# Performance work log

Measured on AMD Instinct MI355X. Metric: run time of the kernel, lower is better.

Reference implementation:

```python
import jax, jax.numpy as jnp
import numpy as np

HID = 32
NUM_GRAPHS = 256
N_NODES = 100000


def graph_conv(x, src, dst, ew, rel_w, rel_b, root_w):
    # PyG GraphConv: out = lin_rel(sum_{j in N(i)} e_ji * x_j) + lin_root(x_i)
    msg = x[src] * ew[:, None]                                  # [E, F] gather
    agg = jax.ops.segment_sum(msg, dst, num_segments=N_NODES)    # [N, F] scatter-add
    return agg @ rel_w + rel_b + x @ root_w


def setup_inputs() -> dict:
    key = jax.random.key(0)
    ks = jax.random.split(key, 16)
    N, E, F = N_NODES, 1600000, 64
    x = jax.random.normal(ks[0], (N, F), dtype=jnp.float32)
    edge_index = jax.random.randint(ks[1], (2, E), 0, N, dtype=jnp.int64)
    edge_attr = jax.random.uniform(ks[2], (E,), dtype=jnp.float32)
    batch = jnp.sort(jax.random.randint(ks[3], (N,), 0, NUM_GRAPHS, dtype=jnp.int64))
    s = lambda k, shp: jax.random.normal(k, shp, dtype=jnp.float32) * 0.1
    return {
        "x": x, "edge_index": edge_index, "edge_attr": edge_attr, "batch": batch,
        "conv1_rel_w": s(ks[4], (F, HID)), "conv1_rel_b": jnp.zeros((HID,), jnp.float32),
        "conv1_root_w": s(ks[5], (F, HID)),
        "conv2_rel_w": s(ks[6], (HID, HID)), "conv2_rel_b": jnp.zeros((HID,), jnp.float32),
        "conv2_root_w": s(ks[7], (HID, HID)),
        "lin1_w": s(ks[8], (HID, 32)), "lin1_b": jnp.zeros((32,), jnp.float32),
        "lin2_w": s(ks[9], (32, 16)), "lin2_b": jnp.zeros((16,), jnp.float32),
        "lin_w": s(ks[10], (16, 1)), "lin_b": jnp.zeros((1,), jnp.float32),
    }


def reference(x, edge_index, edge_attr, batch,
              conv1_rel_w, conv1_rel_b, conv1_root_w,
              conv2_rel_w, conv2_rel_b, conv2_root_w,
              lin1_w, lin1_b, lin2_w, lin2_b, lin_w, lin_b):
    src, dst = edge_index[0], edge_index[1]
    h = jax.nn.relu(graph_conv(x, src, dst, edge_attr, conv1_rel_w, conv1_rel_b, conv1_root_w))
    h = jax.nn.relu(graph_conv(h, src, dst, edge_attr, conv2_rel_w, conv2_rel_b, conv2_root_w))
    # global mean pool over graphs
    sums = jax.ops.segment_sum(h, batch, num_segments=NUM_GRAPHS)          # [G, 32]
    cnts = jax.ops.segment_sum(jnp.ones((h.shape[0],), h.dtype), batch, num_segments=NUM_GRAPHS)
    g = sums / jnp.maximum(cnts, 1.0)[:, None]
    # dropout is identity in eval mode
    g = jax.nn.relu(g @ lin1_w + lin1_b)
    g = g @ lin2_w + lin2_b
    g = jax.nn.relu(g)
    return g @ lin_w + lin_b  # [G, 1]
```

## Files before the change

kernel.cpp:

```cpp
#include <hip/hip_runtime.h>
#include <hip/hip_fp16.h>

#define NGRAPH 256
#define FIN 64
#define HID 32
#define NB_SHIFT 8
#define NB_NODES 256
#define KMAX2 512
#define EPB 2048
#define EPT 8
#define NT 64
#define XPAD 65
#define HPAD 33

__global__ __launch_bounds__(256, 4) void node_lin64(
    const float* __restrict__ x, const float* __restrict__ Wrel,
    const float* __restrict__ Wroot, const float* __restrict__ bias,
    __half* __restrict__ A, float* __restrict__ B, int N)
{
    __shared__ float sWr[FIN * HID];
    __shared__ float sWo[FIN * HID];
    __shared__ float sb[HID];
    __shared__ float sx[NT * XPAD];
    int tid = threadIdx.x;
    {
        const float4* Wr4 = (const float4*)Wrel;
        const float4* Wo4 = (const float4*)Wroot;
        for (int i = tid; i < FIN * HID / 4; i += 256) {
            ((float4*)sWr)[i] = Wr4[i];
            ((float4*)sWo)[i] = Wo4[i];
        }
        if (tid < HID) sb[tid] = bias[tid];
    }
    int base = blockIdx.x * NT;
    {
        const float4* x4 = (const float4*)x;
        for (int i = tid; i < NT * 16; i += 256) {
            int row = i >> 4, c4 = i & 15;
            int n = base + row;
            float4 v = (n < N) ? x4[(size_t)n * 16 + c4]
                               : make_float4(0.f, 0.f, 0.f, 0.f);
            *(float4*)&sx[row * XPAD + c4 * 4] = v;
        }
    }
    __syncthreads();

    int nl = tid >> 3;
    int fq = (tid & 7) * 4;
    const float* xa = &sx[nl * XPAD];
    const float* xb = &sx[(nl + 32) * XPAD];
    float4 ar0 = make_float4(0.f,0.f,0.f,0.f), ao0 = ar0;
    float4 ar1 = ar0, ao1 = ar0;
    #pragma unroll 4
    for (int k = 0; k < FIN; ++k) {
        float4 w4 = *(const float4*)&sWr[k * HID + fq];
        float4 o4 = *(const float4*)&sWo[k * HID + fq];
        float va = xa[k], vb = xb[k];
        ar0.x = fmaf(va, w4.x, ar0.x); ar0.y = fmaf(va, w4.y, ar0.y);
        ar0.z = fmaf(va, w4.z, ar0.z); ar0.w = fmaf(va, w4.w, ar0.w);
        ao0.x = fmaf(va, o4.x, ao0.x); ao0.y = fmaf(va, o4.y, ao0.y);
        ao0.z = fmaf(va, o4.z, ao0.z); ao0.w = fmaf(va, o4.w, ao0.w);
        ar1.x = fmaf(vb, w4.x, ar1.x); ar1.y = fmaf(vb, w4.y, ar1.y);
        ar1.z = fmaf(vb, w4.z, ar1.z); ar1.w = fmaf(vb, w4.w, ar1.w);
        ao1.x = fmaf(vb, o4.x, ao1.x); ao1.y = fmaf(vb, o4.y, ao1.y);
        ao1.z = fmaf(vb, o4.z, ao1.z); ao1.w = fmaf(vb, o4.w, ao1.w);
    }
    float4 bb = *(const float4*)&sb[fq];
    int n0 = base + nl, n1 = base + nl + 32;
    if (n0 < N) {
        __half2 pa = __floats2half2_rn(ar0.x, ar0.y);
        __half2 pb = __floats2half2_rn(ar0.z, ar0.w);
        uint2 pk; pk.x = *(unsigned*)&pa; pk.y = *(unsigned*)&pb;
        *(uint2*)&A[(size_t)n0 * HID + fq] = pk;
        ao0.x += bb.x; ao0.y += bb.y; ao0.z += bb.z; ao0.w += bb.w;
        *(float4*)&B[(size_t)n0 * HID + fq] = ao0;
    }
    if (n1 < N) {
        __half2 pa = __floats2half2_rn(ar1.x, ar1.y);
        __half2 pb = __floats2half2_rn(ar1.z, ar1.w);
        uint2 pk; pk.x = *(unsigned*)&pa; pk.y = *(unsigned*)&pb;
        *(uint2*)&A[(size_t)n1 * HID + fq] = pk;
        ao1.x += bb.x; ao1.y += bb.y; ao1.z += bb.z; ao1.w += bb.w;
        *(float4*)&B[(size_t)n1 * HID + fq] = ao1;
    }
}

__global__ __launch_bounds__(256, 4) void node_lin32(
    const float* __restrict__ Hpre, const float* __restrict__ Wrel,
    const float* __restrict__ Wroot, const float* __restrict__ bias,
    __half* __restrict__ A, float* __restrict__ C, int N)
{
    __shared__ float sWr[HID * HID];
    __shared__ float sWo[HID * HID];
    __shared__ float sb[HID];
    __shared__ float sh[NT * HPAD];
    int tid = threadIdx.x;
    {
        const float4* Wr4 = (const float4*)Wrel;
        const float4* Wo4 = (const float4*)Wroot;
        for (int i = tid; i < HID * HID / 4; i += 256) {
            ((float4*)sWr)[i] = Wr4[i];
            ((float4*)sWo)[i] = Wo4[i];
        }
        if (tid < HID) sb[tid] = bias[tid];
    }
    int base = blockIdx.x * NT;
    {
        const float4* H4 = (const float4*)Hpre;
        for (int i = tid; i < NT * 8; i += 256) {
            int row = i >> 3, c4 = i & 7;
            int n = base + row;
            float4 v = make_float4(0.f, 0.f, 0.f, 0.f);
            if (n < N) {
                v = H4[(size_t)n * 8 + c4];
                v.x = v.x > 0.f ? v.x : 0.f; v.y = v.y > 0.f ? v.y : 0.f;
                v.z = v.z > 0.f ? v.z : 0.f; v.w = v.w > 0.f ? v.w : 0.f;
            }
            *(float4*)&sh[row * HPAD + c4 * 4] = v;
        }
    }
    __syncthreads();

    int nl = tid >> 3;
    int fq = (tid & 7) * 4;
    const float* xa = &sh[nl * HPAD];
    const float* xb = &sh[(nl + 32) * HPAD];
    float4 ar0 = make_float4(0.f,0.f,0.f,0.f), ao0 = ar0;
    float4 ar1 = ar0, ao1 = ar0;
    #pragma unroll 4
    for (int k = 0; k < HID; ++k) {
        float4 w4 = *(const float4*)&sWr[k * HID + fq];
        float4 o4 = *(const float4*)&sWo[k * HID + fq];
        float va = xa[k], vb = xb[k];
        ar0.x = fmaf(va, w4.x, ar0.x); ar0.y = fmaf(va, w4.y, ar0.y);
        ar0.z = fmaf(va, w4.z, ar0.z); ar0.w = fmaf(va, w4.w, ar0.w);
        ao0.x = fmaf(va, o4.x, ao0.x); ao0.y = fmaf(va, o4.y, ao0.y);
        ao0.z = fmaf(va, o4.z, ao0.z); ao0.w = fmaf(va, o4.w, ao0.w);
        ar1.x = fmaf(vb, w4.x, ar1.x); ar1.y = fmaf(vb, w4.y, ar1.y);
        ar1.z = fmaf(vb, w4.z, ar1.z); ar1.w = fmaf(vb, w4.w, ar1.w);
        ao1.x = fmaf(vb, o4.x, ao1.x); ao1.y = fmaf(vb, o4.y, ao1.y);
        ao1.z = fmaf(vb, o4.z, ao1.z); ao1.w = fmaf(vb, o4.w, ao1.w);
    }
    float4 bb = *(const float4*)&sb[fq];
    int n0 = base + nl, n1 = base + nl + 32;
    if (n0 < N) {
        __half2 pa = __floats2half2_rn(ar0.x, ar0.y);
        __half2 pb = __floats2half2_rn(ar0.z, ar0.w);
        uint2 pk; pk.x = *(unsigned*)&pa; pk.y = *(unsigned*)&pb;
        *(uint2*)&A[(size_t)n0 * HID + fq] = pk;
        ao0.x += bb.x; ao0.y += bb.y; ao0.z += bb.z; ao0.w += bb.w;
        *(float4*)&C[(size_t)n0 * HID + fq] = ao0;
    }
    if (n1 < N) {
        __half2 pa = __floats2half2_rn(ar1.x, ar1.y);
        __half2 pb = __floats2half2_rn(ar1.z, ar1.w);
        uint2 pk; pk.x = *(unsigned*)&pa; pk.y = *(unsigned*)&pb;
        *(uint2*)&A[(size_t)n1 * HID + fq] = pk;
        ao1.x += bb.x; ao1.y += bb.y; ao1.z += bb.z; ao1.w += bb.w;
        *(float4*)&C[(size_t)n1 * HID + fq] = ao1;
    }
}


__global__ __launch_bounds__(256) void bucket_hist(
    const int* __restrict__ dst, int* __restrict__ cbb, int E, int K, int NBLK)
{
    __shared__ int h[KMAX2];
    int tid = threadIdx.x;
    for (int i = tid; i < K; i += 256) h[i] = 0;
    __syncthreads();
    int e0 = blockIdx.x * EPB + tid * 8;
    if (e0 + 7 < E) {
        int4 d0 = *reinterpret_cast<const int4*>(dst + e0);
        int4 d1 = *reinterpret_cast<const int4*>(dst + e0 + 4);
        atomicAdd(&h[d0.x >> NB_SHIFT], 1); atomicAdd(&h[d0.y >> NB_SHIFT], 1);
        atomicAdd(&h[d0.z >> NB_SHIFT], 1); atomicAdd(&h[d0.w >> NB_SHIFT], 1);
        atomicAdd(&h[d1.x >> NB_SHIFT], 1); atomicAdd(&h[d1.y >> NB_SHIFT], 1);
        atomicAdd(&h[d1.z >> NB_SHIFT], 1); atomicAdd(&h[d1.w >> NB_SHIFT], 1);
    } else {
        for (int e = e0; e < E && e < e0 + 8; ++e)
            atomicAdd(&h[dst[e] >> NB_SHIFT], 1);
    }
    __syncthreads();
    for (int i = tid; i < K; i += 256)
        cbb[(size_t)i * NBLK + blockIdx.x] = h[i];
}

__global__ __launch_bounds__(256) void bucket_scan(
    int* __restrict__ cbb, int* __restrict__ btot, int NBLK)
{
    __shared__ int sc[256];
    size_t row = (size_t)blockIdx.x * NBLK;
    int t = threadIdx.x;
    int base = t * 4;
    int v[4]; int s = 0;
    #pragma unroll
    for (int j = 0; j < 4; ++j) { v[j] = (base + j < NBLK) ? cbb[row + base + j] : 0; s += v[j]; }
    sc[t] = s;
    __syncthreads();
    int acc = s;
    for (int off = 1; off < 256; off <<= 1) {
        int add = (t >= off) ? sc[t - off] : 0;
        __syncthreads();
        acc += add;
        sc[t] = acc;
        __syncthreads();
    }
    int run = acc - s;
    #pragma unroll
    for (int j = 0; j < 4; ++j) {
        if (base + j < NBLK) cbb[row + base + j] = run;
        run += v[j];
    }
    if (t == 255) btot[blockIdx.x] = acc;
}

__global__ __launch_bounds__(256) void btot_scan(
    const int* __restrict__ btot, int* __restrict__ bbase, int K)
{
    __shared__ int sc[256];
    int t = threadIdx.x;
    int base = t * 4;
    int v[4]; int s = 0;
    #pragma unroll
    for (int j = 0; j < 4; ++j) { v[j] = (base + j < K) ? btot[base + j] : 0; s += v[j]; }
    sc[t] = s;
    __syncthreads();
    int acc = s;
    for (int off = 1; off < 256; off <<= 1) {
        int add = (t >= off) ? sc[t - off] : 0;
        __syncthreads();
        acc += add;
        sc[t] = acc;
        __syncthreads();
    }
    int run = acc - s;
    #pragma unroll
    for (int j = 0; j < 4; ++j) {
        if (base + j < K) bbase[base + j] = run;
        run += v[j];
    }
    if (t == 255) bbase[K] = acc;
}

__global__ __launch_bounds__(256) void partB(
    const int* __restrict__ src, const int* __restrict__ dst,
    const float* __restrict__ ew, const int* __restrict__ cbb,
    const int* __restrict__ bbase, int2* __restrict__ stg8,
    int E, int K, int NBLK)
{
    __shared__ int4 pay[EPB];
    __shared__ int h[KMAX2];
    __shared__ int lofs[KMAX2];
    __shared__ int gb[KMAX2];
    __shared__ int sc[256];
    int tid = threadIdx.x;
    for (int i = tid; i < K; i += 256) h[i] = 0;
    __syncthreads();

    int base = blockIdx.x * EPB;
    int es[EPT], ds[EPT]; float wsr[EPT];
    #pragma unroll
    for (int k = 0; k < EPT; ++k) {
        int e = base + k * 256 + tid;
        if (e < E) {
            es[k] = src[e]; ds[k] = dst[e]; wsr[k] = ew[e];
            atomicAdd(&h[ds[k] >> NB_SHIFT], 1);
        } else ds[k] = -1;
    }
    __syncthreads();

    int b0 = tid * 2;
    int v0 = (b0 < K) ? h[b0] : 0;
    int v1 = (b0 + 1 < K) ? h[b0 + 1] : 0;
    int s = v0 + v1;
    sc[tid] = s;
    __syncthreads();
    int acc = s;
    for (int off = 1; off < 256; off <<= 1) {
        int add = (tid >= off) ? sc[tid - off] : 0;
        __syncthreads();
        acc += add;
        sc[tid] = acc;
        __syncthreads();
    }
    int run = acc - s;
    if (b0 < K) lofs[b0] = run;
    if (b0 + 1 < K) lofs[b0 + 1] = run + v0;
    __syncthreads();

    for (int b = tid; b < K; b += 256) {
        gb[b] = bbase[b] + cbb[(size_t)b * NBLK + blockIdx.x];
        h[b] = lofs[b];
    }
    __syncthreads();

    #pragma unroll
    for (int k = 0; k < EPT; ++k) {
        if (ds[k] >= 0) {
            int b = ds[k] >> NB_SHIFT;
            int dloc = ds[k] & (NB_NODES - 1);
            int slot = atomicAdd(&h[b], 1);
            pay[slot] = make_int4(es[k] | (dloc << 17), __float_as_int(wsr[k]),
                                  gb[b] + slot - lofs[b], 0);
        }
    }
    __syncthreads();

    int tot = E - base; if (tot > EPB) tot = EPB;
    for (int i = tid; i < tot; i += 256) {
        int4 p = pay[i];
        stg8[p.z] = make_int2(p.x, p.y);
    }
}

__global__ __launch_bounds__(512) void partC2(
    const int2* __restrict__ stg8, const int* __restrict__ bbase,
    int* __restrict__ rowptr, int2* __restrict__ perm, int N, int K)
{
    __shared__ int hcnt[NB_NODES];
    __shared__ int hinc[NB_NODES];
    int b = blockIdx.x;
    int n0 = b << NB_SHIFT;
    int nTop = n0 + NB_NODES; if (nTop > N) nTop = N;
    int nloc = nTop - n0;
    int tid = threadIdx.x;
    if (tid < NB_NODES) hcnt[tid] = 0;
    __syncthreads();
    int lo = bbase[b], hi = bbase[b + 1];
    for (int e = lo + tid; e < hi; e += 512)
        atomicAdd(&hcnt[stg8[e].x >> 17], 1);
    __syncthreads();
    if (tid < NB_NODES) hinc[tid] = hcnt[tid];
    __syncthreads();
    for (int off = 1; off < NB_NODES; off <<= 1) {
        int v = (tid < NB_NODES && tid >= off) ? hinc[tid - off] : 0;
        __syncthreads();
        if (tid < NB_NODES) hinc[tid] += v;
        __syncthreads();
    }
    if (tid < nloc) {
        int excl = hinc[tid] - hcnt[tid];
        rowptr[n0 + tid] = lo + excl;
        hcnt[tid] = excl;
    }
    if (b == K - 1 && tid == 0) rowptr[N] = hi;
    __syncthreads();
    for (int e = lo + tid; e < hi; e += 512) {
        int2 p = stg8[e];
        int pos = lo + atomicAdd(&hcnt[p.x >> 17], 1);
        perm[pos] = make_int2(p.x & 0x1FFFF, p.y);
    }
}

__global__ __launch_bounds__(256) void csr_agg(
    const int* __restrict__ rowptr, const int2* __restrict__ perm,
    const __half* __restrict__ A, float* __restrict__ out, int N)
{
    int gid = blockIdx.x * 256 + threadIdx.x;
    int n = gid >> 6;
    if (n >= N) return;
    int lane = threadIdx.x & 63;
    int slot = lane >> 3;
    int q = lane & 7;
    int e0 = rowptr[n], e1 = rowptr[n + 1];
    const uint2* A2 = (const uint2*)A;
    float4 a0 = make_float4(0.f, 0.f, 0.f, 0.f);
    float4 a1 = make_float4(0.f, 0.f, 0.f, 0.f);
    int e = e0 + slot;
    for (; e + 8 < e1; e += 16) {
        int2 p0 = perm[e];
        int2 p1 = perm[e + 8];
        uint2 r0 = A2[(size_t)p0.x * 8 + q];
        uint2 r1 = A2[(size_t)p1.x * 8 + q];
        float w0 = __int_as_float(p0.y), w1 = __int_as_float(p1.y);
        float2 f01 = __half22float2(*(__half2*)&r0.x);
        float2 f23 = __half22float2(*(__half2*)&r0.y);
        float2 g01 = __half22float2(*(__half2*)&r1.x);
        float2 g23 = __half22float2(*(__half2*)&r1.y);
        a0.x = fmaf(f01.x, w0, a0.x); a0.y = fmaf(f01.y, w0, a0.y);
        a0.z = fmaf(f23.x, w0, a0.z); a0.w = fmaf(f23.y, w0, a0.w);
        a1.x = fmaf(g01.x, w1, a1.x); a1.y = fmaf(g01.y, w1, a1.y);
        a1.z = fmaf(g23.x, w1, a1.z); a1.w = fmaf(g23.y, w1, a1.w);
    }
    for (; e < e1; e += 8) {
        int2 p = perm[e];
        uint2 r = A2[(size_t)p.x * 8 + q];
        float w = __int_as_float(p.y);
        float2 f01 = __half22float2(*(__half2*)&r.x);
        float2 f23 = __half22float2(*(__half2*)&r.y);
        a0.x = fmaf(f01.x, w, a0.x); a0.y = fmaf(f01.y, w, a0.y);
        a0.z = fmaf(f23.x, w, a0.z); a0.w = fmaf(f23.y, w, a0.w);
    }
    a0.x += a1.x; a0.y += a1.y; a0.z += a1.z; a0.w += a1.w;
    #pragma unroll
    for (int off = 8; off < 64; off <<= 1) {
        a0.x += __shfl_xor(a0.x, off, 64);
        a0.y += __shfl_xor(a0.y, off, 64);
        a0.z += __shfl_xor(a0.z, off, 64);
        a0.w += __shfl_xor(a0.w, off, 64);
    }
    if (lane < 8) {
        float4* O4 = (float4*)out;
        size_t oi = (size_t)n * 8 + q;
        float4 o = O4[oi];
        o.x += a0.x; o.y += a0.y; o.z += a0.z; o.w += a0.w;
        O4[oi] = o;
    }
}

__global__ __launch_bounds__(256) void pool_mlp(
    const float* __restrict__ C, const int* __restrict__ batch, int N,
    const float* __restrict__ W1, const float* __restrict__ b1,
    const float* __restrict__ W2, const float* __restrict__ b2,
    const float* __restrict__ W3, const float* __restrict__ b3,
    float* __restrict__ out)
{
    int g = blockIdx.x;
    int tid = threadIdx.x;
    int lo, hi;
    {
        int l = 0, r = N;
        while (l < r) { int m = (l + r) >> 1; if (batch[m] < g) l = m + 1; else r = m; }
        lo = l;
        r = N;
        while (l < r) { int m = (l + r) >> 1; if (batch[m] < g + 1) l = m + 1; else r = m; }
        hi = l;
    }
    __shared__ float ssum[8][32];
    __shared__ float gvec[32];
    __shared__ float h1v[32];
    __shared__ float h2v[16];
    int f = tid & 31, seg = tid >> 5;
    float acc = 0.f;
    for (int n = lo + seg; n < hi; n += 8) {
        float v = C[(size_t)n * HID + f];
        acc += v > 0.f ? v : 0.f;
    }
    ssum[seg][f] = acc;
    __syncthreads();
    if (tid < 32) {
        float s = 0.f;
        #pragma unroll
        for (int k = 0; k < 8; ++k) s += ssum[k][tid];
        float c = (float)(hi - lo); c = c > 1.f ? c : 1.f;
        gvec[tid] = s / c;
    }
    __syncthreads();
    if (tid < 32) {
        float a = b1[tid];
        #pragma unroll
        for (int k = 0; k < 32; ++k) a = fmaf(gvec[k], W1[k * 32 + tid], a);
        h1v[tid] = a > 0.f ? a : 0.f;
    }
    __syncthreads();
    if (tid < 16) {
        float a = b2[tid];
        #pragma unroll
        for (int k = 0; k < 32; ++k) a = fmaf(h1v[k], W2[k * 16 + tid], a);
        h2v[tid] = a > 0.f ? a : 0.f;
    }
    __syncthreads();
    if (tid == 0) {
        float o = b3[0];
        #pragma unroll
        for (int k = 0; k < 16; ++k) o = fmaf(h2v[k], W3[k], o);
        out[g] = o;
    }
}

extern "C" void kernel_launch(void* const* d_in, const int* in_sizes, int n_in,
                              void* d_out, int out_size, void* d_ws, size_t ws_size,
                              hipStream_t stream) {
    const float* x     = (const float*)d_in[0];
    const int*   ei    = (const int*)d_in[1];
    const float* ew    = (const float*)d_in[2];
    const int*   batch = (const int*)d_in[3];
    const float* c1rw  = (const float*)d_in[4];
    const float* c1rb  = (const float*)d_in[5];
    const float* c1ow  = (const float*)d_in[6];
    const float* c2rw  = (const float*)d_in[7];
    const float* c2rb  = (const float*)d_in[8];
    const float* c2ow  = (const float*)d_in[9];
    const float* l1w   = (const float*)d_in[10];
    const float* l1b   = (const float*)d_in[11];
    const float* l2w   = (const float*)d_in[12];
    const float* l2b   = (const float*)d_in[13];
    const float* lw    = (const float*)d_in[14];
    const float* lb    = (const float*)d_in[15];

    int N = in_sizes[0] / FIN;
    int E = in_sizes[2];
    const int* src = ei;
    const int* dst = ei + E;
    int K    = (N + NB_NODES - 1) >> NB_SHIFT;
    int NBLK = (E + EPB - 1) / EPB;

    char* ws = (char*)d_ws;
    size_t off = 0;
    auto alloc = [&](size_t nbytes) { void* p = ws + off; off += (nbytes + 255) & ~size_t(255); return p; };
    __half* A     = (__half*)alloc((size_t)N * HID * 2);
    float*  BC    = (float*) alloc((size_t)N * HID * 4);
    int2*   perm  = (int2*)  alloc((size_t)E * 8);
    int*   rowptr = (int*)   alloc((size_t)(N + 1) * 4);
    int*   btot   = (int*)   alloc((size_t)KMAX2 * 4);
    int*   bbase  = (int*)   alloc((size_t)(KMAX2 + 1) * 4);
    int*   cbb    = (int*)A;
    int2*  stg8   = (int2*)BC;

    int nb_node = (N + NT - 1) / NT;
    int nb_agg  = (int)(((long long)N * 64 + 255) / 256);

    bucket_hist<<<NBLK, 256, 0, stream>>>(dst, cbb, E, K, NBLK);
    bucket_scan<<<K, 256, 0, stream>>>(cbb, btot, NBLK);
    btot_scan<<<1, 256, 0, stream>>>(btot, bbase, K);
    partB<<<NBLK, 256, 0, stream>>>(src, dst, ew, cbb, bbase, stg8, E, K, NBLK);
    partC2<<<K, 512, 0, stream>>>(stg8, bbase, rowptr, perm, N, K);

    node_lin64<<<nb_node, 256, 0, stream>>>(x, c1rw, c1ow, c1rb, A, BC, N);
    csr_agg<<<nb_agg, 256, 0, stream>>>(rowptr, perm, A, BC, N);
    node_lin32<<<nb_node, 256, 0, stream>>>(BC, c2rw, c2ow, c2rb, A, BC, N);
    csr_agg<<<nb_agg, 256, 0, stream>>>(rowptr, perm, A, BC, N);
    pool_mlp<<<NGRAPH, 256, 0, stream>>>(BC, batch, N, l1w, l1b, l2w, l2b, lw, lb,
                                         (float*)d_out);
}
```

Before: 173.4 us.

## Fuse layer-1 aggregation with layer-2 node linear and stage partC2 buckets in LDS

Measured after the change: 176.6 us. About the same (+1.8%).

```diff
diff --git a/kernel.cpp b/kernel.cpp
--- a/kernel.cpp
+++ b/kernel.cpp
@@ -11,7 +11,7 @@
 #define EPT 8
 #define NT 64
 #define XPAD 65
-#define HPAD 33
+#define PCAP 6016
 
 __global__ __launch_bounds__(256, 4) void node_lin64(
     const float* __restrict__ x, const float* __restrict__ Wrel,
@@ -85,82 +85,6 @@
     }
 }
 
-__global__ __launch_bounds__(256, 4) void node_lin32(
-    const float* __restrict__ Hpre, const float* __restrict__ Wrel,
-    const float* __restrict__ Wroot, const float* __restrict__ bias,
-    __half* __restrict__ A, float* __restrict__ C, int N)
-{
-    __shared__ float sWr[HID * HID];
-    __shared__ float sWo[HID * HID];
-    __shared__ float sb[HID];
-    __shared__ float sh[NT * HPAD];
-    int tid = threadIdx.x;
-    {
-        const float4* Wr4 = (const float4*)Wrel;
-        const float4* Wo4 = (const float4*)Wroot;
-        for (int i = tid; i < HID * HID / 4; i += 256) {
-            ((float4*)sWr)[i] = Wr4[i];
-            ((float4*)sWo)[i] = Wo4[i];
-        }
-        if (tid < HID) sb[tid] = bias[tid];
-    }
-    int base = blockIdx.x * NT;
-    {
-        const float4* H4 = (const float4*)Hpre;
-        for (int i = tid; i < NT * 8; i += 256) {
-            int row = i >> 3, c4 = i & 7;
-            int n = base + row;
-            float4 v = make_float4(0.f, 0.f, 0.f, 0.f);
-            if (n < N) {
-                v = H4[(size_t)n * 8 + c4];
-                v.x = v.x > 0.f ? v.x : 0.f; v.y = v.y > 0.f ? v.y : 0.f;
-                v.z = v.z > 0.f ? v.z : 0.f; v.w = v.w > 0.f ? v.w : 0.f;
-            }
-            *(float4*)&sh[row * HPAD + c4 * 4] = v;
-        }
-    }
-    __syncthreads();
-
-    int nl = tid >> 3;
-    int fq = (tid & 7) * 4;
-    const float* xa = &sh[nl * HPAD];
-    const float* xb = &sh[(nl + 32) * HPAD];
-    float4 ar0 = make_float4(0.f,0.f,0.f,0.f), ao0 = ar0;
-    float4 ar1 = ar0, ao1 = ar0;
-    #pragma unroll 4
-    for (int k = 0; k < HID; ++k) {
-        float4 w4 = *(const float4*)&sWr[k * HID + fq];
-        float4 o4 = *(const float4*)&sWo[k * HID + fq];
-        float va = xa[k], vb = xb[k];
-        ar0.x = fmaf(va, w4.x, ar0.x); ar0.y = fmaf(va, w4.y, ar0.y);
-        ar0.z = fmaf(va, w4.z, ar0.z); ar0.w = fmaf(va, w4.w, ar0.w);
-        ao0.x = fmaf(va, o4.x, ao0.x); ao0.y = fmaf(va, o4.y, ao0.y);
-        ao0.z = fmaf(va, o4.z, ao0.z); ao0.w = fmaf(va, o4.w, ao0.w);
-        ar1.x = fmaf(vb, w4.x, ar1.x); ar1.y = fmaf(vb, w4.y, ar1.y);
-        ar1.z = fmaf(vb, w4.z, ar1.z); ar1.w = fmaf(vb, w4.w, ar1.w);
-        ao1.x = fmaf(vb, o4.x, ao1.x); ao1.y = fmaf(vb, o4.y, ao1.y);
-        ao1.z = fmaf(vb, o4.z, ao1.z); ao1.w = fmaf(vb, o4.w, ao1.w);
-    }
-    float4 bb = *(const float4*)&sb[fq];
-    int n0 = base + nl, n1 = base + nl + 32;
-    if (n0 < N) {
-        __half2 pa = __floats2half2_rn(ar0.x, ar0.y);
-        __half2 pb = __floats2half2_rn(ar0.z, ar0.w);
-        uint2 pk; pk.x = *(unsigned*)&pa; pk.y = *(unsigned*)&pb;
-        *(uint2*)&A[(size_t)n0 * HID + fq] = pk;
-        ao0.x += bb.x; ao0.y += bb.y; ao0.z += bb.z; ao0.w += bb.w;
-        *(float4*)&C[(size_t)n0 * HID + fq] = ao0;
-    }
-    if (n1 < N) {
-        __half2 pa = __floats2half2_rn(ar1.x, ar1.y);
-        __half2 pb = __floats2half2_rn(ar1.z, ar1.w);
-        uint2 pk; pk.x = *(unsigned*)&pa; pk.y = *(unsigned*)&pb;
-        *(uint2*)&A[(size_t)n1 * HID + fq] = pk;
-        ao1.x += bb.x; ao1.y += bb.y; ao1.z += bb.z; ao1.w += bb.w;
-        *(float4*)&C[(size_t)n1 * HID + fq] = ao1;
-    }
-}
-
 
 __global__ __launch_bounds__(256) void bucket_hist(
     const int* __restrict__ dst, int* __restrict__ cbb, int E, int K, int NBLK)
@@ -318,6 +242,7 @@
     const int2* __restrict__ stg8, const int* __restrict__ bbase,
     int* __restrict__ rowptr, int2* __restrict__ perm, int N, int K)
 {
+    __shared__ int2 pe[PCAP];
     __shared__ int hcnt[NB_NODES];
     __shared__ int hinc[NB_NODES];
     int b = blockIdx.x;
@@ -326,10 +251,20 @@
     int nloc = nTop - n0;
     int tid = threadIdx.x;
     if (tid < NB_NODES) hcnt[tid] = 0;
-    __syncthreads();
     int lo = bbase[b], hi = bbase[b + 1];
-    for (int e = lo + tid; e < hi; e += 512)
-        atomicAdd(&hcnt[stg8[e].x >> 17], 1);
+    int sz = hi - lo;
+    bool fit = (sz <= PCAP);
+    if (fit) {
+        for (int i = tid; i < sz; i += 512) pe[i] = stg8[lo + i];
+    }
+    __syncthreads();
+    if (fit) {
+        for (int i = tid; i < sz; i += 512)
+            atomicAdd(&hcnt[pe[i].x >> 17], 1);
+    } else {
+        for (int e = lo + tid; e < hi; e += 512)
+            atomicAdd(&hcnt[stg8[e].x >> 17], 1);
+    }
     __syncthreads();
     if (tid < NB_NODES) hinc[tid] = hcnt[tid];
     __syncthreads();
@@ -346,10 +281,113 @@
     }
     if (b == K - 1 && tid == 0) rowptr[N] = hi;
     __syncthreads();
-    for (int e = lo + tid; e < hi; e += 512) {
-        int2 p = stg8[e];
-        int pos = lo + atomicAdd(&hcnt[p.x >> 17], 1);
-        perm[pos] = make_int2(p.x & 0x1FFFF, p.y);
+    if (fit) {
+        for (int i = tid; i < sz; i += 512) {
+            int2 p = pe[i];
+            int pos = lo + atomicAdd(&hcnt[p.x >> 17], 1);
+            perm[pos] = make_int2(p.x & 0x1FFFF, p.y);
+        }
+    } else {
+        for (int e = lo + tid; e < hi; e += 512) {
+            int2 p = stg8[e];
+            int pos = lo + atomicAdd(&hcnt[p.x >> 17], 1);
+            perm[pos] = make_int2(p.x & 0x1FFFF, p.y);
+        }
+    }
+}
+
+__global__ __launch_bounds__(256) void csr_agg_lin32(
+    const int* __restrict__ rowptr, const int2* __restrict__ perm,
+    const __half* __restrict__ A1, const float* __restrict__ Bbase,
+    const float* __restrict__ W2rel, const float* __restrict__ W2root,
+    const float* __restrict__ b2,
+    __half* __restrict__ A2, float* __restrict__ C2base, int N)
+{
+    __shared__ float sWr[HID * HID];
+    __shared__ float sWo[HID * HID];
+    __shared__ float sb2[HID];
+    __shared__ float hrow[4][HID];
+    int tid = threadIdx.x;
+    {
+        const float4* Wr4 = (const float4*)W2rel;
+        const float4* Wo4 = (const float4*)W2root;
+        for (int i = tid; i < HID * HID / 4; i += 256) {
+            ((float4*)sWr)[i] = Wr4[i];
+            ((float4*)sWo)[i] = Wo4[i];
+        }
+        if (tid < HID) sb2[tid] = b2[tid];
+    }
+    __syncthreads();
+
+    int gid = blockIdx.x * 256 + tid;
+    int n = gid >> 6;
+    int w = tid >> 6;
+    int lane = tid & 63;
+    bool active = (n < N);
+
+    float4 a0 = make_float4(0.f, 0.f, 0.f, 0.f);
+    float4 a1 = make_float4(0.f, 0.f, 0.f, 0.f);
+    int slot = lane >> 3, q = lane & 7;
+    if (active) {
+        int e0 = rowptr[n], e1 = rowptr[n + 1];
+        const uint2* A2p = (const uint2*)A1;
+        int e = e0 + slot;
+        for (; e + 8 < e1; e += 16) {
+            int2 p0 = perm[e];
+            int2 p1 = perm[e + 8];
+            uint2 r0 = A2p[(size_t)p0.x * 8 + q];
+            uint2 r1 = A2p[(size_t)p1.x * 8 + q];
+            float w0 = __int_as_float(p0.y), w1 = __int_as_float(p1.y);
+            float2 f01 = __half22float2(*(__half2*)&r0.x);
+            float2 f23 = __half22float2(*(__half2*)&r0.y);
+            float2 g01 = __half22float2(*(__half2*)&r1.x);
+            float2 g23 = __half22float2(*(__half2*)&r1.y);
+            a0.x = fmaf(f01.x, w0, a0.x); a0.y = fmaf(f01.y, w0, a0.y);
+            a0.z = fmaf(f23.x, w0, a0.z); a0.w = fmaf(f23.y, w0, a0.w);
+            a1.x = fmaf(g01.x, w1, a1.x); a1.y = fmaf(g01.y, w1, a1.y);
+            a1.z = fmaf(g23.x, w1, a1.z); a1.w = fmaf(g23.y, w1, a1.w);
+        }
+        for (; e < e1; e += 8) {
+            int2 p = perm[e];
+            uint2 r = A2p[(size_t)p.x * 8 + q];
+            float wv = __int_as_float(p.y);
+            float2 f01 = __half22float2(*(__half2*)&r.x);
+            float2 f23 = __half22float2(*(__half2*)&r.y);
+            a0.x = fmaf(f01.x, wv, a0.x); a0.y = fmaf(f01.y, wv, a0.y);
+            a0.z = fmaf(f23.x, wv, a0.z); a0.w = fmaf(f23.y, wv, a0.w);
+        }
+        a0.x += a1.x; a0.y += a1.y; a0.z += a1.z; a0.w += a1.w;
+        #pragma unroll
+        for (int off = 8; off < 64; off <<= 1) {
+            a0.x += __shfl_xor(a0.x, off, 64);
+            a0.y += __shfl_xor(a0.y, off, 64);
+            a0.z += __shfl_xor(a0.z, off, 64);
+            a0.w += __shfl_xor(a0.w, off, 64);
+        }
+        if (lane < 8) {
+            float4 o = ((const float4*)Bbase)[(size_t)n * 8 + q];
+            o.x += a0.x; o.y += a0.y; o.z += a0.z; o.w += a0.w;
+            o.x = o.x > 0.f ? o.x : 0.f; o.y = o.y > 0.f ? o.y : 0.f;
+            o.z = o.z > 0.f ? o.z : 0.f; o.w = o.w > 0.f ? o.w : 0.f;
+            *(float4*)&hrow[w][q * 4] = o;
+        }
+    }
+    __syncthreads();
+    if (active) {
+        int f = lane & 31;
+        bool isRel = lane < 32;
+        const float* W = isRel ? sWr : sWo;
+        float a = isRel ? 0.f : sb2[f];
+        #pragma unroll 8
+        for (int k4 = 0; k4 < HID; k4 += 4) {
+            float4 h4 = *(const float4*)&hrow[w][k4];
+            a = fmaf(h4.x, W[(k4 + 0) * HID + f], a);
+            a = fmaf(h4.y, W[(k4 + 1) * HID + f], a);
+            a = fmaf(h4.z, W[(k4 + 2) * HID + f], a);
+            a = fmaf(h4.w, W[(k4 + 3) * HID + f], a);
+        }
+        if (isRel) A2[((size_t)n << 5) + f] = __float2half(a);
+        else       C2base[((size_t)n << 5) + f] = a;
     }
 }
 
@@ -499,13 +537,14 @@
     char* ws = (char*)d_ws;
     size_t off = 0;
     auto alloc = [&](size_t nbytes) { void* p = ws + off; off += (nbytes + 255) & ~size_t(255); return p; };
-    __half* A     = (__half*)alloc((size_t)N * HID * 2);
+    __half* A1    = (__half*)alloc((size_t)N * HID * 2);
+    __half* A2    = (__half*)alloc((size_t)N * HID * 2);
     float*  BC    = (float*) alloc((size_t)N * HID * 4);
     int2*   perm  = (int2*)  alloc((size_t)E * 8);
     int*   rowptr = (int*)   alloc((size_t)(N + 1) * 4);
     int*   btot   = (int*)   alloc((size_t)KMAX2 * 4);
     int*   bbase  = (int*)   alloc((size_t)(KMAX2 + 1) * 4);
-    int*   cbb    = (int*)A;
+    int*   cbb    = (int*)A1;
     int2*  stg8   = (int2*)BC;
 
     int nb_node = (N + NT - 1) / NT;
@@ -517,10 +556,10 @@
     partB<<<NBLK, 256, 0, stream>>>(src, dst, ew, cbb, bbase, stg8, E, K, NBLK);
     partC2<<<K, 512, 0, stream>>>(stg8, bbase, rowptr, perm, N, K);
 
-    node_lin64<<<nb_node, 256, 0, stream>>>(x, c1rw, c1ow, c1rb, A, BC, N);
-    csr_agg<<<nb_agg, 256, 0, stream>>>(rowptr, perm, A, BC, N);
-    node_lin32<<<nb_node, 256, 0, stream>>>(BC, c2rw, c2ow, c2rb, A, BC, N);
-    csr_agg<<<nb_agg, 256, 0, stream>>>(rowptr, perm, A, BC, N);
+    node_lin64<<<nb_node, 256, 0, stream>>>(x, c1rw, c1ow, c1rb, A1, BC, N);
+    csr_agg_lin32<<<nb_agg, 256, 0, stream>>>(rowptr, perm, A1, BC,
+                                              c2rw, c2ow, c2rb, A2, BC, N);
+    csr_agg<<<nb_agg, 256, 0, stream>>>(rowptr, perm, A2, BC, N);
     pool_mlp<<<NGRAPH, 256, 0, stream>>>(BC, batch, N, l1w, l1b, l2w, l2b, lw, lb,
                                          (float*)d_out);
 }
```

## Stage bucket edges in LDS for partC2 and widen csr_agg gathers to 16 bytes

Applied to the files above, without the earlier changes.

After: 177.5 us. +2.3%, slower.

```diff
diff --git a/kernel.cpp b/kernel.cpp
--- a/kernel.cpp
+++ b/kernel.cpp
@@ -12,6 +12,7 @@
 #define NT 64
 #define XPAD 65
 #define HPAD 33
+#define PCAP 6016
 
 __global__ __launch_bounds__(256, 4) void node_lin64(
     const float* __restrict__ x, const float* __restrict__ Wrel,
@@ -318,6 +319,7 @@
     const int2* __restrict__ stg8, const int* __restrict__ bbase,
     int* __restrict__ rowptr, int2* __restrict__ perm, int N, int K)
 {
+    __shared__ int2 pe[PCAP];
     __shared__ int hcnt[NB_NODES];
     __shared__ int hinc[NB_NODES];
     int b = blockIdx.x;
@@ -326,10 +328,20 @@
     int nloc = nTop - n0;
     int tid = threadIdx.x;
     if (tid < NB_NODES) hcnt[tid] = 0;
-    __syncthreads();
     int lo = bbase[b], hi = bbase[b + 1];
-    for (int e = lo + tid; e < hi; e += 512)
-        atomicAdd(&hcnt[stg8[e].x >> 17], 1);
+    int sz = hi - lo;
+    bool fit = (sz <= PCAP);
+    if (fit) {
+        for (int i = tid; i < sz; i += 512) pe[i] = stg8[lo + i];
+    }
+    __syncthreads();
+    if (fit) {
+        for (int i = tid; i < sz; i += 512)
+            atomicAdd(&hcnt[pe[i].x >> 17], 1);
+    } else {
+        for (int e = lo + tid; e < hi; e += 512)
+            atomicAdd(&hcnt[stg8[e].x >> 17], 1);
+    }
     __syncthreads();
     if (tid < NB_NODES) hinc[tid] = hcnt[tid];
     __syncthreads();
@@ -346,10 +358,18 @@
     }
     if (b == K - 1 && tid == 0) rowptr[N] = hi;
     __syncthreads();
-    for (int e = lo + tid; e < hi; e += 512) {
-        int2 p = stg8[e];
-        int pos = lo + atomicAdd(&hcnt[p.x >> 17], 1);
-        perm[pos] = make_int2(p.x & 0x1FFFF, p.y);
+    if (fit) {
+        for (int i = tid; i < sz; i += 512) {
+            int2 p = pe[i];
+            int pos = lo + atomicAdd(&hcnt[p.x >> 17], 1);
+            perm[pos] = make_int2(p.x & 0x1FFFF, p.y);
+        }
+    } else {
+        for (int e = lo + tid; e < hi; e += 512) {
+            int2 p = stg8[e];
+            int pos = lo + atomicAdd(&hcnt[p.x >> 17], 1);
+            perm[pos] = make_int2(p.x & 0x1FFFF, p.y);
+        }
     }
 }
 
@@ -361,51 +381,65 @@
     int n = gid >> 6;
     if (n >= N) return;
     int lane = threadIdx.x & 63;
-    int slot = lane >> 3;
-    int q = lane & 7;
+    int slot = lane >> 2;
+    int q = lane & 3;
     int e0 = rowptr[n], e1 = rowptr[n + 1];
-    const uint2* A2 = (const uint2*)A;
-    float4 a0 = make_float4(0.f, 0.f, 0.f, 0.f);
-    float4 a1 = make_float4(0.f, 0.f, 0.f, 0.f);
+    const uint4* A4 = (const uint4*)A;
+    float a0[8] = {0.f,0.f,0.f,0.f,0.f,0.f,0.f,0.f};
+    float a1[8] = {0.f,0.f,0.f,0.f,0.f,0.f,0.f,0.f};
     int e = e0 + slot;
-    for (; e + 8 < e1; e += 16) {
+    for (; e + 16 < e1; e += 32) {
         int2 p0 = perm[e];
-        int2 p1 = perm[e + 8];
-        uint2 r0 = A2[(size_t)p0.x * 8 + q];
-        uint2 r1 = A2[(size_t)p1.x * 8 + q];
+        int2 p1 = perm[e + 16];
+        uint4 r0 = A4[(size_t)p0.x * 4 + q];
+        uint4 r1 = A4[(size_t)p1.x * 4 + q];
         float w0 = __int_as_float(p0.y), w1 = __int_as_float(p1.y);
-        float2 f01 = __half22float2(*(__half2*)&r0.x);
-        float2 f23 = __half22float2(*(__half2*)&r0.y);
-        float2 g01 = __half22float2(*(__half2*)&r1.x);
-        float2 g23 = __half22float2(*(__half2*)&r1.y);
-        a0.x = fmaf(f01.x, w0, a0.x); a0.y = fmaf(f01.y, w0, a0.y);
-        a0.z = fmaf(f23.x, w0, a0.z); a0.w = fmaf(f23.y, w0, a0.w);
-        a1.x = fmaf(g01.x, w1, a1.x); a1.y = fmaf(g01.y, w1, a1.y);
-        a1.z = fmaf(g23.x, w1, a1.z); a1.w = fmaf(g23.y, w1, a1.w);
-    }
-    for (; e < e1; e += 8) {
+        float2 c0 = __half22float2(*(__half2*)&r0.x);
+        float2 c1 = __half22float2(*(__half2*)&r0.y);
+        float2 c2 = __half22float2(*(__half2*)&r0.z);
+        float2 c3 = __half22float2(*(__half2*)&r0.w);
+        a0[0] = fmaf(c0.x, w0, a0[0]); a0[1] = fmaf(c0.y, w0, a0[1]);
+        a0[2] = fmaf(c1.x, w0, a0[2]); a0[3] = fmaf(c1.y, w0, a0[3]);
+        a0[4] = fmaf(c2.x, w0, a0[4]); a0[5] = fmaf(c2.y, w0, a0[5]);
+        a0[6] = fmaf(c3.x, w0, a0[6]); a0[7] = fmaf(c3.y, w0, a0[7]);
+        float2 d0 = __half22float2(*(__half2*)&r1.x);
+        float2 d1 = __half22float2(*(__half2*)&r1.y);
+        float2 d2 = __half22float2(*(__half2*)&r1.z);
+        float2 d3 = __half22float2(*(__half2*)&r1.w);
+        a1[0] = fmaf(d0.x, w1, a1[0]); a1[1] = fmaf(d0.y, w1, a1[1]);
+        a1[2] = fmaf(d1.x, w1, a1[2]); a1[3] = fmaf(d1.y, w1, a1[3]);
+        a1[4] = fmaf(d2.x, w1, a1[4]); a1[5] = fmaf(d2.y, w1, a1[5]);
+        a1[6] = fmaf(d3.x, w1, a1[6]); a1[7] = fmaf(d3.y, w1, a1[7]);
+    }
+    for (; e < e1; e += 16) {
         int2 p = perm[e];
-        uint2 r = A2[(size_t)p.x * 8 + q];
+        uint4 r = A4[(size_t)p.x * 4 + q];
         float w = __int_as_float(p.y);
-        float2 f01 = __half22float2(*(__half2*)&r.x);
-        float2 f23 = __half22float2(*(__half2*)&r.y);
-        a0.x = fmaf(f01.x, w, a0.x); a0.y = fmaf(f01.y, w, a0.y);
-        a0.z = fmaf(f23.x, w, a0.z); a0.w = fmaf(f23.y, w, a0.w);
-    }
-    a0.x += a1.x; a0.y += a1.y; a0.z += a1.z; a0.w += a1.w;
-    #pragma unroll
-    for (int off = 8; off < 64; off <<= 1) {
-        a0.x += __shfl_xor(a0.x, off, 64);
-        a0.y += __shfl_xor(a0.y, off, 64);
-        a0.z += __shfl_xor(a0.z, off, 64);
-        a0.w += __shfl_xor(a0.w, off, 64);
-    }
-    if (lane < 8) {
+        float2 c0 = __half22float2(*(__half2*)&r.x);
+        float2 c1 = __half22float2(*(__half2*)&r.y);
+        float2 c2 = __half22float2(*(__half2*)&r.z);
+        float2 c3 = __half22float2(*(__half2*)&r.w);
+        a0[0] = fmaf(c0.x, w, a0[0]); a0[1] = fmaf(c0.y, w, a0[1]);
+        a0[2] = fmaf(c1.x, w, a0[2]); a0[3] = fmaf(c1.y, w, a0[3]);
+        a0[4] = fmaf(c2.x, w, a0[4]); a0[5] = fmaf(c2.y, w, a0[5]);
+        a0[6] = fmaf(c3.x, w, a0[6]); a0[7] = fmaf(c3.y, w, a0[7]);
+    }
+    #pragma unroll
+    for (int i = 0; i < 8; ++i) a0[i] += a1[i];
+    #pragma unroll
+    for (int off = 4; off < 64; off <<= 1) {
+        #pragma unroll
+        for (int i = 0; i < 8; ++i) a0[i] += __shfl_xor(a0[i], off, 64);
+    }
+    if (lane < 4) {
         float4* O4 = (float4*)out;
-        size_t oi = (size_t)n * 8 + q;
+        size_t oi = (size_t)n * 8 + q * 2;
         float4 o = O4[oi];
-        o.x += a0.x; o.y += a0.y; o.z += a0.z; o.w += a0.w;
+        o.x += a0[0]; o.y += a0[1]; o.z += a0[2]; o.w += a0[3];
         O4[oi] = o;
+        float4 p = O4[oi + 1];
+        p.x += a0[4]; p.y += a0[5]; p.z += a0[6]; p.w += a0[7];
+        O4[oi + 1] = p;
     }
 }
 
```

## Split fp16 gather table into two feature halves and stage bucket in LDS

Applied to the files above, without the earlier changes.

After: 274.2 us. 1.58x slower.

```diff
diff --git a/kernel.cpp b/kernel.cpp
--- a/kernel.cpp
+++ b/kernel.cpp
@@ -12,6 +12,8 @@
 #define NT 64
 #define XPAD 65
 #define HPAD 33
+#define PCAP 6016
+
 
 __global__ __launch_bounds__(256, 4) void node_lin64(
     const float* __restrict__ x, const float* __restrict__ Wrel,
@@ -66,12 +68,14 @@
         ao1.z = fmaf(vb, o4.z, ao1.z); ao1.w = fmaf(vb, o4.w, ao1.w);
     }
     float4 bb = *(const float4*)&sb[fq];
+    size_t tOff = (fq < 16) ? (size_t)0 : (size_t)N * 16;
+    int fl = fq & 15;
     int n0 = base + nl, n1 = base + nl + 32;
     if (n0 < N) {
         __half2 pa = __floats2half2_rn(ar0.x, ar0.y);
         __half2 pb = __floats2half2_rn(ar0.z, ar0.w);
         uint2 pk; pk.x = *(unsigned*)&pa; pk.y = *(unsigned*)&pb;
-        *(uint2*)&A[(size_t)n0 * HID + fq] = pk;
+        *(uint2*)&A[tOff + (size_t)n0 * 16 + fl] = pk;
         ao0.x += bb.x; ao0.y += bb.y; ao0.z += bb.z; ao0.w += bb.w;
         *(float4*)&B[(size_t)n0 * HID + fq] = ao0;
     }
@@ -79,7 +83,7 @@
         __half2 pa = __floats2half2_rn(ar1.x, ar1.y);
         __half2 pb = __floats2half2_rn(ar1.z, ar1.w);
         uint2 pk; pk.x = *(unsigned*)&pa; pk.y = *(unsigned*)&pb;
-        *(uint2*)&A[(size_t)n1 * HID + fq] = pk;
+        *(uint2*)&A[tOff + (size_t)n1 * 16 + fl] = pk;
         ao1.x += bb.x; ao1.y += bb.y; ao1.z += bb.z; ao1.w += bb.w;
         *(float4*)&B[(size_t)n1 * HID + fq] = ao1;
     }
@@ -142,12 +146,14 @@
         ao1.z = fmaf(vb, o4.z, ao1.z); ao1.w = fmaf(vb, o4.w, ao1.w);
     }
     float4 bb = *(const float4*)&sb[fq];
+    size_t tOff = (fq < 16) ? (size_t)0 : (size_t)N * 16;
+    int fl = fq & 15;
     int n0 = base + nl, n1 = base + nl + 32;
     if (n0 < N) {
         __half2 pa = __floats2half2_rn(ar0.x, ar0.y);
         __half2 pb = __floats2half2_rn(ar0.z, ar0.w);
         uint2 pk; pk.x = *(unsigned*)&pa; pk.y = *(unsigned*)&pb;
-        *(uint2*)&A[(size_t)n0 * HID + fq] = pk;
+        *(uint2*)&A[tOff + (size_t)n0 * 16 + fl] = pk;
         ao0.x += bb.x; ao0.y += bb.y; ao0.z += bb.z; ao0.w += bb.w;
         *(float4*)&C[(size_t)n0 * HID + fq] = ao0;
     }
@@ -155,7 +161,7 @@
         __half2 pa = __floats2half2_rn(ar1.x, ar1.y);
         __half2 pb = __floats2half2_rn(ar1.z, ar1.w);
         uint2 pk; pk.x = *(unsigned*)&pa; pk.y = *(unsigned*)&pb;
-        *(uint2*)&A[(size_t)n1 * HID + fq] = pk;
+        *(uint2*)&A[tOff + (size_t)n1 * 16 + fl] = pk;
         ao1.x += bb.x; ao1.y += bb.y; ao1.z += bb.z; ao1.w += bb.w;
         *(float4*)&C[(size_t)n1 * HID + fq] = ao1;
     }
@@ -318,6 +324,7 @@
     const int2* __restrict__ stg8, const int* __restrict__ bbase,
     int* __restrict__ rowptr, int2* __restrict__ perm, int N, int K)
 {
+    __shared__ int2 pe[PCAP];
     __shared__ int hcnt[NB_NODES];
     __shared__ int hinc[NB_NODES];
     int b = blockIdx.x;
@@ -326,10 +333,20 @@
     int nloc = nTop - n0;
     int tid = threadIdx.x;
     if (tid < NB_NODES) hcnt[tid] = 0;
-    __syncthreads();
     int lo = bbase[b], hi = bbase[b + 1];
-    for (int e = lo + tid; e < hi; e += 512)
-        atomicAdd(&hcnt[stg8[e].x >> 17], 1);
+    int sz = hi - lo;
+    bool fit = (sz <= PCAP);
+    if (fit) {
+        for (int i = tid; i < sz; i += 512) pe[i] = stg8[lo + i];
+    }
+    __syncthreads();
+    if (fit) {
+        for (int i = tid; i < sz; i += 512)
+            atomicAdd(&hcnt[pe[i].x >> 17], 1);
+    } else {
+        for (int e = lo + tid; e < hi; e += 512)
+            atomicAdd(&hcnt[stg8[e].x >> 17], 1);
+    }
     __syncthreads();
     if (tid < NB_NODES) hinc[tid] = hcnt[tid];
     __syncthreads();
@@ -346,16 +363,24 @@
     }
     if (b == K - 1 && tid == 0) rowptr[N] = hi;
     __syncthreads();
-    for (int e = lo + tid; e < hi; e += 512) {
-        int2 p = stg8[e];
-        int pos = lo + atomicAdd(&hcnt[p.x >> 17], 1);
-        perm[pos] = make_int2(p.x & 0x1FFFF, p.y);
-    }
-}
-
-__global__ __launch_bounds__(256) void csr_agg(
+    if (fit) {
+        for (int i = tid; i < sz; i += 512) {
+            int2 p = pe[i];
+            int pos = lo + atomicAdd(&hcnt[p.x >> 17], 1);
+            perm[pos] = make_int2(p.x & 0x1FFFF, p.y);
+        }
+    } else {
+        for (int e = lo + tid; e < hi; e += 512) {
+            int2 p = stg8[e];
+            int pos = lo + atomicAdd(&hcnt[p.x >> 17], 1);
+            perm[pos] = make_int2(p.x & 0x1FFFF, p.y);
+        }
+    }
+}
+
+__global__ __launch_bounds__(256) void csr_agg_half(
     const int* __restrict__ rowptr, const int2* __restrict__ perm,
-    const __half* __restrict__ A, float* __restrict__ out, int N)
+    const __half* __restrict__ tab, float* __restrict__ out, int N, int half)
 {
     int gid = blockIdx.x * 256 + threadIdx.x;
     int n = gid >> 6;
@@ -364,48 +389,43 @@
     int slot = lane >> 3;
     int q = lane & 7;
     int e0 = rowptr[n], e1 = rowptr[n + 1];
-    const uint2* A2 = (const uint2*)A;
-    float4 a0 = make_float4(0.f, 0.f, 0.f, 0.f);
-    float4 a1 = make_float4(0.f, 0.f, 0.f, 0.f);
+    const unsigned* T = (const unsigned*)tab;
+    float ax0 = 0.f, ay0 = 0.f, ax1 = 0.f, ay1 = 0.f;
+    const long long* P = (const long long*)perm;
     int e = e0 + slot;
     for (; e + 8 < e1; e += 16) {
-        int2 p0 = perm[e];
-        int2 p1 = perm[e + 8];
-        uint2 r0 = A2[(size_t)p0.x * 8 + q];
-        uint2 r1 = A2[(size_t)p1.x * 8 + q];
-        float w0 = __int_as_float(p0.y), w1 = __int_as_float(p1.y);
-        float2 f01 = __half22float2(*(__half2*)&r0.x);
-        float2 f23 = __half22float2(*(__half2*)&r0.y);
-        float2 g01 = __half22float2(*(__half2*)&r1.x);
-        float2 g23 = __half22float2(*(__half2*)&r1.y);
-        a0.x = fmaf(f01.x, w0, a0.x); a0.y = fmaf(f01.y, w0, a0.y);
-        a0.z = fmaf(f23.x, w0, a0.z); a0.w = fmaf(f23.y, w0, a0.w);
-        a1.x = fmaf(g01.x, w1, a1.x); a1.y = fmaf(g01.y, w1, a1.y);
-        a1.z = fmaf(g23.x, w1, a1.z); a1.w = fmaf(g23.y, w1, a1.w);
+        long long pv0 = __builtin_nontemporal_load(&P[e]);
+        long long pv1 = __builtin_nontemporal_load(&P[e + 8]);
+        int s0 = (int)(unsigned)pv0, s1 = (int)(unsigned)pv1;
+        float w0 = __int_as_float((int)(pv0 >> 32));
+        float w1 = __int_as_float((int)(pv1 >> 32));
+        unsigned r0 = T[(size_t)s0 * 8 + q];
+        unsigned r1 = T[(size_t)s1 * 8 + q];
+        float2 f0 = __half22float2(*(__half2*)&r0);
+        float2 f1 = __half22float2(*(__half2*)&r1);
+        ax0 = fmaf(f0.x, w0, ax0); ay0 = fmaf(f0.y, w0, ay0);
+        ax1 = fmaf(f1.x, w1, ax1); ay1 = fmaf(f1.y, w1, ay1);
     }
     for (; e < e1; e += 8) {
-        int2 p = perm[e];
-        uint2 r = A2[(size_t)p.x * 8 + q];
-        float w = __int_as_float(p.y);
-        float2 f01 = __half22float2(*(__half2*)&r.x);
-        float2 f23 = __half22float2(*(__half2*)&r.y);
-        a0.x = fmaf(f01.x, w, a0.x); a0.y = fmaf(f01.y, w, a0.y);
-        a0.z = fmaf(f23.x, w, a0.z); a0.w = fmaf(f23.y, w, a0.w);
-    }
-    a0.x += a1.x; a0.y += a1.y; a0.z += a1.z; a0.w += a1.w;
+        long long pv = __builtin_nontemporal_load(&P[e]);
+        int s = (int)(unsigned)pv;
+        float w = __int_as_float((int)(pv >> 32));
+        unsigned r = T[(size_t)s * 8 + q];
+        float2 f = __half22float2(*(__half2*)&r);
+        ax0 = fmaf(f.x, w, ax0); ay0 = fmaf(f.y, w, ay0);
+    }
+    ax0 += ax1; ay0 += ay1;
     #pragma unroll
     for (int off = 8; off < 64; off <<= 1) {
-        a0.x += __shfl_xor(a0.x, off, 64);
-        a0.y += __shfl_xor(a0.y, off, 64);
-        a0.z += __shfl_xor(a0.z, off, 64);
-        a0.w += __shfl_xor(a0.w, off, 64);
+        ax0 += __shfl_xor(ax0, off, 64);
+        ay0 += __shfl_xor(ay0, off, 64);
     }
     if (lane < 8) {
-        float4* O4 = (float4*)out;
-        size_t oi = (size_t)n * 8 + q;
-        float4 o = O4[oi];
-        o.x += a0.x; o.y += a0.y; o.z += a0.z; o.w += a0.w;
-        O4[oi] = o;
+        float* O = out + (size_t)n * HID + half * 16 + q * 2;
+        float o0 = __builtin_nontemporal_load(&O[0]);
+        float o1 = __builtin_nontemporal_load(&O[1]);
+        __builtin_nontemporal_store(o0 + ax0, &O[0]);
+        __builtin_nontemporal_store(o1 + ay0, &O[1]);
     }
 }
 
@@ -508,6 +528,9 @@
     int*   cbb    = (int*)A;
     int2*  stg8   = (int2*)BC;
 
+    __half* A0 = A;
+    __half* A1 = A + (size_t)N * 16;
+
     int nb_node = (N + NT - 1) / NT;
     int nb_agg  = (int)(((long long)N * 64 + 255) / 256);
 
@@ -518,9 +541,11 @@
     partC2<<<K, 512, 0, stream>>>(stg8, bbase, rowptr, perm, N, K);
 
     node_lin64<<<nb_node, 256, 0, stream>>>(x, c1rw, c1ow, c1rb, A, BC, N);
-    csr_agg<<<nb_agg, 256, 0, stream>>>(rowptr, perm, A, BC, N);
+    csr_agg_half<<<nb_agg, 256, 0, stream>>>(rowptr, perm, A0, BC, N, 0);
+    csr_agg_half<<<nb_agg, 256, 0, stream>>>(rowptr, perm, A1, BC, N, 1);
     node_lin32<<<nb_node, 256, 0, stream>>>(BC, c2rw, c2ow, c2rb, A, BC, N);
-    csr_agg<<<nb_agg, 256, 0, stream>>>(rowptr, perm, A, BC, N);
+    csr_agg_half<<<nb_agg, 256, 0, stream>>>(rowptr, perm, A0, BC, N, 0);
+    csr_agg_half<<<nb_agg, 256, 0, stream>>>(rowptr, perm, A1, BC, N, 1);
     pool_mlp<<<NGRAPH, 256, 0, stream>>>(BC, batch, N, l1w, l1b, l2w, l2b, lw, lb,
                                          (float*)d_out);
 }
```
